# Kernel tuning notes

Hardware: AMD Instinct MI355X
Metric: run time of the kernel (lower is better)

## Reference

```python
import jax, jax.numpy as jnp
import numpy as np

B, S, E, H, D, NE, R = 2, 2048, 2048, 16, 128, 8, 16
HALF = D // 2
THETA = 10000.0


def setup_inputs() -> dict:
    key = jax.random.key(0)
    ks = jax.random.split(key, 18)

    def w(k, shape, fan_in):
        return jax.random.normal(k, shape, jnp.float32) / np.float32(np.sqrt(fan_in))

    inp = {
        "x": jax.random.normal(ks[0], (B, S, E), jnp.float32),
        "expert_mask": jax.random.uniform(ks[1], (B, S, NE), dtype=jnp.float32),
    }
    for i, n in enumerate(("q", "k", "v")):
        inp["W" + n] = w(ks[2 + 3 * i], (H * D, E), E)
        inp["b" + n] = jnp.zeros((H * D,), jnp.float32)
        inp["A" + n] = w(ks[3 + 3 * i], (NE, R, E), E)
        inp["B" + n] = w(ks[4 + 3 * i], (H * D, NE, R), R)
    inp["Wo"] = w(ks[11], (E, H * D), H * D)
    inp["bo"] = jnp.zeros((E,), jnp.float32)
    inp["Ao"] = w(ks[12], (NE, R, H * D), H * D)
    inp["Bo"] = w(ks[13], (E, NE, R), R)
    return inp


def routed_linear(x, W, b, A, Bm, mask):
    """MaybeRoutedLinear: dense base + expert-routed low-rank path gated by mask [B,S,NE]."""
    y = jnp.einsum("bsi,oi->bso", x, W) + b
    h = jnp.einsum("bsi,eri->bser", x, A) * mask[..., None]  # [B,S,NE,R]
    return y + jnp.einsum("bser,oer->bso", h, Bm)


def apply_rope(t):
    """Llama-style rotary embedding. t: [B,S,H,D]."""
    inv_freq = 1.0 / (THETA ** (jnp.arange(0, D, 2, dtype=jnp.float32) / D))  # [D/2]
    freqs = jnp.arange(S, dtype=jnp.float32)[:, None] * inv_freq[None, :]  # [S,D/2]
    cos = jnp.concatenate([jnp.cos(freqs)] * 2, -1)[None, :, None, :]  # [1,S,1,D]
    sin = jnp.concatenate([jnp.sin(freqs)] * 2, -1)[None, :, None, :]
    rot = jnp.concatenate([-t[..., HALF:], t[..., :HALF]], -1)
    return t * cos + rot * sin


def reference(x, expert_mask, Wq, bq, Aq, Bq, Wk, bk, Ak, Bk, Wv, bv, Av, Bv, Wo, bo, Ao, Bo):
    q = routed_linear(x, Wq, bq, Aq, Bq, expert_mask).reshape(B, S, H, D)
    k = routed_linear(x, Wk, bk, Ak, Bk, expert_mask).reshape(B, S, H, D)
    v = routed_linear(x, Wv, bv, Av, Bv, expert_mask).reshape(B, S, H, D)
    q = apply_rope(q)
    k = apply_rope(k)
    scores = jnp.einsum("bqhd,bkhd->bhqk", q, k) / jnp.float32(np.sqrt(D))
    causal = jnp.tril(jnp.ones((S, S), dtype=bool))
    scores = jnp.where(causal[None, None], scores, jnp.finfo(scores.dtype).min)
    probs = jax.nn.softmax(scores, axis=-1)
    o = jnp.einsum("bhqk,bkhd->bqhd", probs, v).reshape(B, S, H * D)
    return routed_linear(o, Wo, bo, Ao, Bo, expert_mask)
```

## Files before the change

### kernel.cpp

```cpp
#include <hip/hip_runtime.h>


#define B_ 2
#define S_ 2048
#define E_ 2048
#define H_ 16
#define D_ 128
#define NE_ 8
#define R_ 16
#define HD_ 2048
#define M_ 4096
#define KL_ 128

typedef unsigned short u16;
typedef unsigned int u32;
typedef __attribute__((ext_vector_type(8))) short bf16x8;
typedef __attribute__((ext_vector_type(4))) float f32x4;

typedef const __attribute__((address_space(1))) void gvoid_t;
typedef __attribute__((address_space(3))) void svoid_t;

__device__ __forceinline__ float bf2f(u16 u) {
    union { u32 i; float f; } v; v.i = ((u32)u) << 16; return v.f;
}
__device__ __forceinline__ u16 f2bf(float f) {
    union { float f; u32 i; } v; v.f = f;
    u32 x = v.i;
    return (u16)((x + 0x7fffu + ((x >> 16) & 1u)) >> 16);
}
__device__ __forceinline__ float ldf(const void* p, size_t i, int f) {
    return f ? ((const float*)p)[i] : bf2f(((const u16*)p)[i]);
}
__device__ __forceinline__ float4 ld4(const void* p, size_t i, int f) {
    if (f) return *(const float4*)((const float*)p + i);
    ushort4 v = *(const ushort4*)((const u16*)p + i);
    return make_float4(bf2f(v.x), bf2f(v.y), bf2f(v.z), bf2f(v.w));
}

__global__ void k_detect(const void* __restrict__ x, int* __restrict__ flags) {
    __shared__ int votes[2];
    int tid = threadIdx.x;
    if (tid < 2) votes[tid] = 0;
    __syncthreads();
    const u32* p = (const u32*)x;
    int bad = 0, tot = 0;
    for (int i = tid; i < 4096; i += 64) {
        u32 lo = p[i] & 0xffffu;
        if (lo) {
            tot++;
            int e = (int)((lo >> 7) & 0xffu);
            if (e < 100 || e > 150) bad++;
        }
    }
    atomicAdd(&votes[0], bad);
    atomicAdd(&votes[1], tot);
    __syncthreads();
    if (tid == 0) flags[0] = (votes[1] > 0 && votes[0] * 10 > votes[1] * 3) ? 1 : 0;
}

__global__ void k_cvt(const void* __restrict__ src, u16* __restrict__ dst, int n,
                      const int* __restrict__ flags) {
    int fin = flags[0];
    int i = (blockIdx.x * 256 + threadIdx.x) * 4;
    if (i >= n) return;
    float4 v = ld4(src, i, fin);
    ushort4 o;
    o.x = f2bf(v.x); o.y = f2bf(v.y); o.z = f2bf(v.z); o.w = f2bf(v.w);
    *(ushort4*)(dst + i) = o;
}

#define NX_  8388608L
#define NA1_ 262144L
#define NW_  4194304L
__global__ void k_cvt_all(
    const void* __restrict__ x,
    const void* __restrict__ Aq, const void* __restrict__ Ak,
    const void* __restrict__ Av, const void* __restrict__ Ao,
    const void* __restrict__ Bq, const void* __restrict__ Bk,
    const void* __restrict__ Bv, const void* __restrict__ Bo,
    const void* __restrict__ Wq, const void* __restrict__ Wk,
    const void* __restrict__ Wv,
    u16* __restrict__ Xb, u16* __restrict__ Acat, u16* __restrict__ Bmcat,
    u16* __restrict__ Wqb, u16* __restrict__ Wkb, u16* __restrict__ Wvb,
    const int* __restrict__ flags) {
    int fin = flags[0];
    long i = (long)(blockIdx.x * 256 + threadIdx.x) * 4;
    const void* src; u16* dst; long off;
    if (i < NX_) { src = x; dst = Xb; off = i; }
    else if (i < NX_ + 4 * NA1_) {
        long j = i - NX_; int p = (int)(j >> 18); off = j & (NA1_ - 1);
        src = (p == 0) ? Aq : (p == 1) ? Ak : (p == 2) ? Av : Ao;
        dst = Acat + (long)p * NA1_;
    } else if (i < NX_ + 8 * NA1_) {
        long j = i - NX_ - 4 * NA1_; int p = (int)(j >> 18); off = j & (NA1_ - 1);
        src = (p == 0) ? Bq : (p == 1) ? Bk : (p == 2) ? Bv : Bo;
        dst = Bmcat + (long)p * NA1_;
    } else {
        long j = i - NX_ - 8 * NA1_; int p = (int)(j / NW_); off = j - (long)p * NW_;
        src = (p == 0) ? Wq : (p == 1) ? Wk : Wv;
        dst = (p == 0) ? Wqb : (p == 1) ? Wkb : Wvb;
    }
    float4 v = ld4(src, off, fin);
    ushort4 o;
    o.x = f2bf(v.x); o.y = f2bf(v.y); o.z = f2bf(v.z); o.w = f2bf(v.w);
    *(ushort4*)(dst + off) = o;
}

#define BM_ 128
#define BN_ 128
#define BK_ 64

__global__ __launch_bounds__(256, 2) void k_gemm_mfma(
    const u16* __restrict__ A, int lda,
    const u16* __restrict__ Bw, int ldb, int K1,
    const u16* __restrict__ A2, int lda2,
    const u16* __restrict__ B2, int K2,
    const void* __restrict__ bias, const void* __restrict__ mask,
    void* __restrict__ C, int ldc, int store_mode,
    const int* __restrict__ flags) {
    __shared__ __align__(16) u16 As[BM_ * BK_];
    __shared__ __align__(16) u16 Bs[BN_ * BK_];
    int fin = flags[0];
    int tid = threadIdx.x;
    int w = tid >> 6, lane = tid & 63;
    int l15 = lane & 15, quad = lane >> 4;
    int wm = w >> 1, wn = w & 1;
    int m0 = blockIdx.y * BM_, n0 = blockIdx.x * BN_;
    int lrow = lane >> 3;
    int lcol = (lane & 7) * 8;

    f32x4 acc[4][4];
#pragma unroll
    for (int mt = 0; mt < 4; mt++)
#pragma unroll
        for (int nt = 0; nt < 4; nt++)
#pragma unroll
            for (int r = 0; r < 4; r++) acc[mt][nt][r] = 0.f;

    int n1 = K1 / BK_, n2 = K2 / BK_;
    int total = n1 + n2;
    for (int it = 0; it < total; it++) {
        const u16 *pa, *pb; int sa, sb, kb;
        if (it < n1) { pa = A;  sa = lda;  pb = Bw; sb = ldb; kb = it * BK_; }
        else         { pa = A2; sa = lda2; pb = B2; sb = K2;  kb = (it - n1) * BK_; }
        __syncthreads();
#pragma unroll
        for (int i = 0; i < 4; i++) {
            int rowb = (w * 4 + i) * 8;
            int r = rowb + lrow;
            __builtin_amdgcn_global_load_lds(
                (gvoid_t*)(pa + (size_t)(m0 + r) * sa + kb + lcol),
                (svoid_t*)(As + rowb * BK_), 16, 0, 0);
            __builtin_amdgcn_global_load_lds(
                (gvoid_t*)(pb + (size_t)(n0 + r) * sb + kb + lcol),
                (svoid_t*)(Bs + rowb * BK_), 16, 0, 0);
        }
        __syncthreads();
#pragma unroll
        for (int kk = 0; kk < 2; kk++) {
            int ko = kk * 32 + quad * 8;
            bf16x8 af[4], bf[4];
#pragma unroll
            for (int mt = 0; mt < 4; mt++)
                af[mt] = *(const bf16x8*)(As + (wm * 64 + mt * 16 + l15) * BK_ + ko);
#pragma unroll
            for (int nt = 0; nt < 4; nt++)
                bf[nt] = *(const bf16x8*)(Bs + (wn * 64 + nt * 16 + l15) * BK_ + ko);
#pragma unroll
            for (int mt = 0; mt < 4; mt++)
#pragma unroll
                for (int nt = 0; nt < 4; nt++)
                    acc[mt][nt] = __builtin_amdgcn_mfma_f32_16x16x32_bf16(
                        af[mt], bf[nt], acc[mt][nt], 0, 0, 0);
        }
    }

#pragma unroll
    for (int mt = 0; mt < 4; mt++) {
#pragma unroll
        for (int r = 0; r < 4; r++) {
            int m = m0 + wm * 64 + mt * 16 + quad * 4 + r;
#pragma unroll
            for (int nt = 0; nt < 4; nt++) {
                int n = n0 + wn * 64 + nt * 16 + l15;
                float v = acc[mt][nt][r];
                if (bias) v += ldf(bias, (size_t)n, fin);
                if (mask) v *= ldf(mask, (size_t)m * NE_ + ((n & 127) >> 4), fin);
                int f32out = (store_mode == 2) ? fin : store_mode;
                if (f32out) ((float*)C)[(size_t)m * ldc + n] = v;
                else        ((u16*)C)[(size_t)m * ldc + n] = f2bf(v);
            }
        }
    }
}

__global__ void k_rope2(u16* __restrict__ Q, u16* __restrict__ K) {
    const int n = M_ * HD_ / 2;
    int idx = blockIdx.x * 256 + threadIdx.x;
    u16* Y = (idx < n) ? Q : K;
    int id = (idx < n) ? idx : idx - n;
    int d2 = id & 63;
    int sh = id >> 6;
    int s = (sh >> 4) & (S_ - 1);
    float inv = powf(10000.f, -(float)d2 * (1.f / 64.f));
    float fr = (float)s * inv;
    float c, sn;
    sincosf(fr, &sn, &c);
    size_t base = ((size_t)sh) << 7;
    float t0 = bf2f(Y[base + d2]);
    float t1 = bf2f(Y[base + d2 + 64]);
    Y[base + d2]      = f2bf(t0 * c - t1 * sn);
    Y[base + d2 + 64] = f2bf(t1 * c + t0 * sn);
}

__global__ void k_transpose_v(const u16* __restrict__ Vb, u16* __restrict__ Vt) {
    __shared__ u16 t[32][33];
    int s0 = blockIdx.x * 32;
    int n0 = blockIdx.y * 32;
    int b  = blockIdx.z;
    int tx = threadIdx.x & 31, ty = threadIdx.x >> 5;
#pragma unroll
    for (int r = 0; r < 4; r++)
        t[ty + r * 8][tx] = Vb[((size_t)(b * S_ + s0 + ty + r * 8)) * HD_ + n0 + tx];
    __syncthreads();
#pragma unroll
    for (int r = 0; r < 4; r++)
        Vt[((size_t)(b * HD_ + n0 + ty + r * 8)) * S_ + s0 + tx] = t[tx][ty + r * 8];
}

#define KS_ST 136
#define VT_ST 72
#define SCALE_ 0.088388347648318447f

__global__ __launch_bounds__(256, 3) void k_flash6(
    const u16* __restrict__ Q, const u16* __restrict__ K,
    const u16* __restrict__ Vt, u16* __restrict__ O) {
    __shared__ __align__(16) u16 Ks[64 * KS_ST];
    __shared__ __align__(16) u16 Vs[128 * VT_ST];
    __shared__ __align__(16) u16 Ps[64 * VT_ST];
    int tid = threadIdx.x;
    int w = tid >> 6, lane = tid & 63;
    int l15 = lane & 15, quad = lane >> 4;
    int bh = blockIdx.y, b = bh >> 4, h = bh & 15;
    int t = 31 - blockIdx.x;
    int q0 = t * 64;

    int krow[4], kd8[4], vd[4], vkg[4];
#pragma unroll
    for (int it = 0; it < 4; it++) {
        int idx = it * 256 + tid;
        krow[it] = idx >> 4; kd8[it] = (idx & 15) * 8;
        vd[it] = idx >> 3;   vkg[it] = (idx & 7) * 8;
    }

    bf16x8 qf[4];
    size_t baseQ = ((size_t)(b * S_ + q0 + w * 16 + l15)) * HD_ + h * D_;
#pragma unroll
    for (int ks = 0; ks < 4; ks++)
        qf[ks] = *(const bf16x8*)(Q + baseQ + ks * 32 + quad * 8);

    f32x4 of[8];
#pragma unroll
    for (int nt = 0; nt < 8; nt++)
#pragma unroll
        for (int r = 0; r < 4; r++) of[nt][r] = 0.f;
    float mreg = -30000.f, lreg = 0.f;
    int qrow = q0 + w * 16 + l15;

    int nch = t + 1;

    bf16x8 kpre[4], vpre[4];
#pragma unroll
    for (int it = 0; it < 4; it++) {
        kpre[it] = *(const bf16x8*)(K + ((size_t)(b * S_ + krow[it])) * HD_ + h * D_ + kd8[it]);
        vpre[it] = *(const bf16x8*)(Vt + ((size_t)(bh * 128 + vd[it])) * S_ + vkg[it]);
    }

    for (int c = 0; c < nch; c++) {
        int k0 = c * 64;
        __syncthreads();
#pragma unroll
        for (int it = 0; it < 4; it++) {
            *(bf16x8*)(Ks + krow[it] * KS_ST + kd8[it]) = kpre[it];
            *(bf16x8*)(Vs + vd[it] * VT_ST + vkg[it]) = vpre[it];
        }
        __syncthreads();
        if (c + 1 < nch) {
            int k1 = k0 + 64;
#pragma unroll
            for (int it = 0; it < 4; it++) {
                kpre[it] = *(const bf16x8*)(K + ((size_t)(b * S_ + k1 + krow[it])) * HD_ + h * D_ + kd8[it]);
                vpre[it] = *(const bf16x8*)(Vt + ((size_t)(bh * 128 + vd[it])) * S_ + k1 + vkg[it]);
            }
        }

        f32x4 sf[4];
#pragma unroll
        for (int nt = 0; nt < 4; nt++)
#pragma unroll
            for (int r = 0; r < 4; r++) sf[nt][r] = 0.f;
#pragma unroll
        for (int ks = 0; ks < 4; ks++) {
            int koff = ks * 32 + quad * 8;
            bf16x8 qa = qf[ks];
#pragma unroll
            for (int nt = 0; nt < 4; nt++) {
                bf16x8 kb = *(const bf16x8*)(Ks + (nt * 16 + l15) * KS_ST + koff);
                sf[nt] = __builtin_amdgcn_mfma_f32_16x16x32_bf16(kb, qa, sf[nt], 0, 0, 0);
            }
        }

#pragma unroll
        for (int nt = 0; nt < 4; nt++) {
            int keyb = k0 + nt * 16 + quad * 4;
#pragma unroll
            for (int r = 0; r < 4; r++) {
                float sv = sf[nt][r] * SCALE_;
                sf[nt][r] = (keyb + r > qrow) ? -30000.f : sv;
            }
        }

        float t0 = fmaxf(fmaxf(sf[0][0], sf[0][1]), fmaxf(sf[0][2], sf[0][3]));
        float t1 = fmaxf(fmaxf(sf[1][0], sf[1][1]), fmaxf(sf[1][2], sf[1][3]));
        float t2 = fmaxf(fmaxf(sf[2][0], sf[2][1]), fmaxf(sf[2][2], sf[2][3]));
        float t3 = fmaxf(fmaxf(sf[3][0], sf[3][1]), fmaxf(sf[3][2], sf[3][3]));
        float cmax = fmaxf(fmaxf(t0, t1), fmaxf(t2, t3));
        cmax = fmaxf(cmax, __shfl_xor(cmax, 16, 64));
        cmax = fmaxf(cmax, __shfl_xor(cmax, 32, 64));
        float mnew = fmaxf(mreg, cmax);
        float a = __expf(mreg - mnew);
        mreg = mnew;
#pragma unroll
        for (int nt = 0; nt < 4; nt++)
#pragma unroll
            for (int r = 0; r < 4; r++)
                sf[nt][r] = __expf(sf[nt][r] - mnew);
        float s0 = (sf[0][0] + sf[0][1]) + (sf[0][2] + sf[0][3]);
        float s1 = (sf[1][0] + sf[1][1]) + (sf[1][2] + sf[1][3]);
        float s2 = (sf[2][0] + sf[2][1]) + (sf[2][2] + sf[2][3]);
        float s3 = (sf[3][0] + sf[3][1]) + (sf[3][2] + sf[3][3]);
        float psum = (s0 + s1) + (s2 + s3);
        psum += __shfl_xor(psum, 16, 64);
        psum += __shfl_xor(psum, 32, 64);
        lreg = lreg * a + psum;

        float al[4];
#pragma unroll
        for (int r = 0; r < 4; r++) al[r] = __shfl(a, quad * 4 + r, 16);

#pragma unroll
        for (int nt = 0; nt < 4; nt++)
#pragma unroll
            for (int r = 0; r < 4; r++)
                Ps[(w * 16 + l15) * VT_ST + nt * 16 + quad * 4 + r] = f2bf(sf[nt][r]);
#pragma unroll
        for (int nt = 0; nt < 8; nt++)
#pragma unroll
            for (int r = 0; r < 4; r++) of[nt][r] *= al[r];

#pragma unroll
        for (int ks2 = 0; ks2 < 2; ks2++) {
            int koff = ks2 * 32 + quad * 8;
            bf16x8 pa = *(const bf16x8*)(Ps + (w * 16 + l15) * VT_ST + koff);
#pragma unroll
            for (int nt = 0; nt < 8; nt++) {
                bf16x8 vb = *(const bf16x8*)(Vs + (nt * 16 + l15) * VT_ST + koff);
                of[nt] = __builtin_amdgcn_mfma_f32_16x16x32_bf16(pa, vb, of[nt], 0, 0, 0);
            }
        }
    }

    float linv = 1.f / lreg;
    float inv[4];
#pragma unroll
    for (int r = 0; r < 4; r++) inv[r] = __shfl(linv, quad * 4 + r, 16);
    int rowb = q0 + w * 16 + quad * 4;
#pragma unroll
    for (int r = 0; r < 4; r++) {
        size_t base = ((size_t)(b * S_ + rowb + r)) * HD_ + h * D_;
#pragma unroll
        for (int nt = 0; nt < 8; nt++)
            O[base + nt * 16 + l15] = f2bf(of[nt][r] * inv[r]);
    }
}

extern "C" void kernel_launch(void* const* d_in, const int* in_sizes, int n_in,
                              void* d_out, int out_size, void* d_ws, size_t ws_size,
                              hipStream_t stream) {
    const void* x    = d_in[0];
    const void* mask = d_in[1];
    const void* Wq = d_in[2];  const void* bq = d_in[3];
    const void* Aq = d_in[4];  const void* Bq = d_in[5];
    const void* Wk = d_in[6];  const void* bk = d_in[7];
    const void* Ak = d_in[8];  const void* Bk = d_in[9];
    const void* Wv = d_in[10]; const void* bv = d_in[11];
    const void* Av = d_in[12]; const void* Bv = d_in[13];
    const void* Wo = d_in[14]; const void* bo = d_in[15];
    const void* Ao = d_in[16]; const void* Bo = d_in[17];

    char* ws = (char*)d_ws;
    const long MB = 1 << 20;
    int* flags = (int*)ws;
    u16* Xb    = (u16*)(ws + 1  * MB);
    u16* Acat  = (u16*)(ws + 17 * MB);
    u16* Bmcat = (u16*)(ws + 19 * MB);
    u16* hg3   = (u16*)(ws + 21 * MB);
    u16* hgo   = (u16*)(ws + 24 * MB);
    u16* Qb    = (u16*)(ws + 25 * MB);
    u16* Kb    = (u16*)(ws + 41 * MB);
    u16* Vb    = (u16*)(ws + 57 * MB);
    u16* Vt    = (u16*)(ws + 73 * MB);
    u16* Wqb   = Kb;
    u16* Wkb   = Vb;
    u16* Wvb   = Vt;
    u16* Wob   = Qb;
    u16* Ob    = Vb;

    k_detect<<<1, 64, 0, stream>>>(x, flags);
    const long NCVT = NX_ + 8 * NA1_ + 3 * NW_;
    k_cvt_all<<<NCVT / 1024, 256, 0, stream>>>(
        x, Aq, Ak, Av, Ao, Bq, Bk, Bv, Bo, Wq, Wk, Wv,
        Xb, Acat, Bmcat, Wqb, Wkb, Wvb, flags);

    k_gemm_mfma<<<dim3(3, M_ / BM_), 256, 0, stream>>>(
        Xb, E_, Acat, E_, E_, nullptr, 0, nullptr, 0,
        nullptr, mask, hg3, 384, 0, flags);

    dim3 gg(HD_ / BN_, M_ / BM_);
    k_gemm_mfma<<<gg, 256, 0, stream>>>(Xb, E_, Wqb, E_, E_, hg3 + 0,   384, Bmcat, KL_,
                                        bq, nullptr, Qb, HD_, 0, flags);
    k_gemm_mfma<<<gg, 256, 0, stream>>>(Xb, E_, Wkb, E_, E_, hg3 + 128, 384, Bmcat + NA1_, KL_,
                                        bk, nullptr, Kb, HD_, 0, flags);
    k_gemm_mfma<<<gg, 256, 0, stream>>>(Xb, E_, Wvb, E_, E_, hg3 + 256, 384, Bmcat + 2 * NA1_, KL_,
                                        bv, nullptr, Vb, HD_, 0, flags);

    k_rope2<<<(M_ * HD_) / 256, 256, 0, stream>>>(Qb, Kb);
    k_transpose_v<<<dim3(S_ / 32, HD_ / 32, B_), 256, 0, stream>>>(Vb, Vt);

    k_flash6<<<dim3(32, 32), 256, 0, stream>>>(Qb, Kb, Vt, Ob);

    k_cvt<<<NW_ / 1024, 256, 0, stream>>>(Wo, Wob, (int)NW_, flags);
    k_gemm_mfma<<<dim3(1, M_ / BM_), 256, 0, stream>>>(
        Ob, HD_, Acat + 3 * NA1_, E_, E_, nullptr, 0, nullptr, 0,
        nullptr, mask, hgo, KL_, 0, flags);
    k_gemm_mfma<<<gg, 256, 0, stream>>>(Ob, HD_, Wob, E_, E_, hgo, KL_, Bmcat + 3 * NA1_, KL_,
                                        bo, nullptr, d_out, HD_, 2, flags);
}
```

Before: 723.3 us.

## Fuse QKV projections into one 256x256-tile GEMM with 4-stage LDS pipeline

Replaces the three separate Q/K/V projection GEMMs with a single launch of a new 256x256-tile, 512-thread MFMA kernel. The kernel reads a concatenated bf16 weight buffer, chooses the per-projection bias and low-rank operands from the column block, and scatters into the Q/K/V outputs. It prefetches 4 stages through direct global-to-LDS loads with explicit vmcnt waits and uses a grouped tile swizzle. The output projection also switches to this kernel. The larger tiles are meant to raise operand reuse and cut launch count, at the cost of about 128KB of LDS per block (so roughly one block per CU) and only 128 blocks for the output GEMM, which may leave many CUs idle.

Result: slower. 798.5 us (+10.4%).

```diff
diff --git a/kernel.cpp b/kernel.cpp
--- a/kernel.cpp
+++ b/kernel.cpp
@@ -81,7 +81,7 @@
     const void* __restrict__ Wq, const void* __restrict__ Wk,
     const void* __restrict__ Wv,
     u16* __restrict__ Xb, u16* __restrict__ Acat, u16* __restrict__ Bmcat,
-    u16* __restrict__ Wqb, u16* __restrict__ Wkb, u16* __restrict__ Wvb,
+    u16* __restrict__ Wcat,
     const int* __restrict__ flags) {
     int fin = flags[0];
     long i = (long)(blockIdx.x * 256 + threadIdx.x) * 4;
@@ -98,7 +98,7 @@
     } else {
         long j = i - NX_ - 8 * NA1_; int p = (int)(j / NW_); off = j - (long)p * NW_;
         src = (p == 0) ? Wq : (p == 1) ? Wk : Wv;
-        dst = (p == 0) ? Wqb : (p == 1) ? Wkb : Wvb;
+        dst = Wcat + (long)p * NW_;
     }
     float4 v = ld4(src, off, fin);
     ushort4 o;
@@ -194,6 +194,130 @@
     }
 }
 
+#define GBM 256
+#define GBN 256
+#define GBK 32
+
+__global__ __launch_bounds__(512, 2) void k_gemm256(
+    const u16* __restrict__ A, int lda,
+    const u16* __restrict__ Bw, int ldb, int K1,
+    const u16* __restrict__ A2, int lda2,
+    const u16* __restrict__ B2, int K2,
+    const void* __restrict__ bias0, const void* __restrict__ bias1,
+    const void* __restrict__ bias2,
+    void* __restrict__ C, int ldc, int store_mode,
+    const int* __restrict__ flags) {
+    __shared__ __align__(16) u16 As[4][GBM * GBK];
+    __shared__ __align__(16) u16 Bs[4][GBN * GBK];
+    int fin = flags[0];
+    int tid = threadIdx.x;
+    int w = tid >> 6, lane = tid & 63;
+    int l15 = lane & 15, quad = lane >> 4;
+    int wm = w >> 2, wn = w & 3;
+
+    int nxt = gridDim.x;
+    int lin = blockIdx.y * gridDim.x + blockIdx.x;
+    int cpx = (gridDim.x * gridDim.y) >> 3;
+    int wg = (lin & 7) * cpx + (lin >> 3);
+    int m0 = (wg / nxt) * GBM;
+    int n0 = (wg % nxt) * GBN;
+
+    int p = (store_mode == 3) ? (n0 >> 11) : 0;
+    const u16* A2p = A2 + p * 128;
+    const u16* B2p = B2 + (long)p * NA1_;
+    int nloc = (store_mode == 3) ? (n0 & 2047) : n0;
+
+    int srow = tid >> 2;
+    int scol = (tid & 3) * 8;
+    int nk1 = K1 >> 5;
+    int NT = nk1 + (K2 >> 5);
+
+    f32x4 acc[8][4];
+#pragma unroll
+    for (int mt = 0; mt < 8; mt++)
+#pragma unroll
+        for (int nt = 0; nt < 4; nt++)
+#pragma unroll
+            for (int r = 0; r < 4; r++) acc[mt][nt][r] = 0.f;
+
+    auto stage = [&](int kt) {
+        const u16 *pa, *pb; int sa, sb, kb, nb;
+        if (kt < nk1) { pa = A;   sa = lda;  pb = Bw;  sb = ldb; kb = kt * GBK; nb = n0; }
+        else          { pa = A2p; sa = lda2; pb = B2p; sb = K2;  kb = (kt - nk1) * GBK; nb = nloc; }
+        int buf = kt & 3;
+#pragma unroll
+        for (int j = 0; j < 2; j++) {
+            __builtin_amdgcn_global_load_lds(
+                (gvoid_t*)(pa + (size_t)(m0 + j * 128 + srow) * sa + kb + scol),
+                (svoid_t*)(&As[buf][(j * 128 + w * 16) * GBK]), 16, 0, 0);
+            __builtin_amdgcn_global_load_lds(
+                (gvoid_t*)(pb + (size_t)(nb + j * 128 + srow) * sb + kb + scol),
+                (svoid_t*)(&Bs[buf][(j * 128 + w * 16) * GBK]), 16, 0, 0);
+        }
+    };
+
+    stage(0);
+    if (NT > 1) stage(1);
+    if (NT > 2) stage(2);
+
+    for (int kt = 0; kt < NT; kt++) {
+        int buf = kt & 3;
+        if (kt + 3 < NT) {
+            stage(kt + 3);
+            asm volatile("s_waitcnt vmcnt(12)" ::: "memory");
+        } else {
+            int rem = NT - 1 - kt;
+            if (rem >= 2)      asm volatile("s_waitcnt vmcnt(8)" ::: "memory");
+            else if (rem == 1) asm volatile("s_waitcnt vmcnt(4)" ::: "memory");
+            else               asm volatile("s_waitcnt vmcnt(0)" ::: "memory");
+        }
+        __builtin_amdgcn_s_barrier();
+        __builtin_amdgcn_sched_barrier(0);
+
+        bf16x8 af[8], bfr[4];
+#pragma unroll
+        for (int mt = 0; mt < 8; mt++)
+            af[mt] = *(const bf16x8*)(&As[buf][(wm * 128 + mt * 16 + l15) * GBK + quad * 8]);
+#pragma unroll
+        for (int nt = 0; nt < 4; nt++)
+            bfr[nt] = *(const bf16x8*)(&Bs[buf][(wn * 64 + nt * 16 + l15) * GBK + quad * 8]);
+
+        __builtin_amdgcn_s_setprio(1);
+#pragma unroll
+        for (int mt = 0; mt < 8; mt++)
+#pragma unroll
+            for (int nt = 0; nt < 4; nt++)
+                acc[mt][nt] = __builtin_amdgcn_mfma_f32_16x16x32_bf16(
+                    af[mt], bfr[nt], acc[mt][nt], 0, 0, 0);
+        __builtin_amdgcn_s_setprio(0);
+
+        __builtin_amdgcn_s_barrier();
+        __builtin_amdgcn_sched_barrier(0);
+    }
+
+    const void* bp = (store_mode == 3) ? (p == 0 ? bias0 : p == 1 ? bias1 : bias2)
+                                       : bias0;
+#pragma unroll
+    for (int mt = 0; mt < 8; mt++) {
+#pragma unroll
+        for (int r = 0; r < 4; r++) {
+            int m = m0 + wm * 128 + mt * 16 + quad * 4 + r;
+#pragma unroll
+            for (int nt = 0; nt < 4; nt++) {
+                int n = n0 + wn * 64 + nt * 16 + l15;
+                float v = acc[mt][nt][r];
+                if (bp) v += ldf(bp, (size_t)(n & 2047), fin);
+                if (store_mode == 3) {
+                    ((u16*)C)[(size_t)p * 8388608 + (size_t)m * 2048 + (n & 2047)] = f2bf(v);
+                } else {
+                    if (fin) ((float*)C)[(size_t)m * ldc + n] = v;
+                    else     ((u16*)C)[(size_t)m * ldc + n] = f2bf(v);
+                }
+            }
+        }
+    }
+}
+
 __global__ void k_rope2(u16* __restrict__ Q, u16* __restrict__ K) {
     const int n = M_ * HD_ / 2;
     int idx = blockIdx.x * 256 + threadIdx.x;
@@ -410,9 +534,7 @@
     u16* Kb    = (u16*)(ws + 41 * MB);
     u16* Vb    = (u16*)(ws + 57 * MB);
     u16* Vt    = (u16*)(ws + 73 * MB);
-    u16* Wqb   = Kb;
-    u16* Wkb   = Vb;
-    u16* Wvb   = Vt;
+    u16* Wcat  = (u16*)(ws + 73 * MB);
     u16* Wob   = Qb;
     u16* Ob    = Vb;
 
@@ -420,19 +542,15 @@
     const long NCVT = NX_ + 8 * NA1_ + 3 * NW_;
     k_cvt_all<<<NCVT / 1024, 256, 0, stream>>>(
         x, Aq, Ak, Av, Ao, Bq, Bk, Bv, Bo, Wq, Wk, Wv,
-        Xb, Acat, Bmcat, Wqb, Wkb, Wvb, flags);
+        Xb, Acat, Bmcat, Wcat, flags);
 
     k_gemm_mfma<<<dim3(3, M_ / BM_), 256, 0, stream>>>(
         Xb, E_, Acat, E_, E_, nullptr, 0, nullptr, 0,
         nullptr, mask, hg3, 384, 0, flags);
 
-    dim3 gg(HD_ / BN_, M_ / BM_);
-    k_gemm_mfma<<<gg, 256, 0, stream>>>(Xb, E_, Wqb, E_, E_, hg3 + 0,   384, Bmcat, KL_,
-                                        bq, nullptr, Qb, HD_, 0, flags);
-    k_gemm_mfma<<<gg, 256, 0, stream>>>(Xb, E_, Wkb, E_, E_, hg3 + 128, 384, Bmcat + NA1_, KL_,
-                                        bk, nullptr, Kb, HD_, 0, flags);
-    k_gemm_mfma<<<gg, 256, 0, stream>>>(Xb, E_, Wvb, E_, E_, hg3 + 256, 384, Bmcat + 2 * NA1_, KL_,
-                                        bv, nullptr, Vb, HD_, 0, flags);
+    k_gemm256<<<dim3(6144 / GBN, M_ / GBM), 512, 0, stream>>>(
+        Xb, E_, Wcat, E_, E_, hg3, 384, Bmcat, KL_,
+        bq, bk, bv, Qb, HD_, 3, flags);
 
     k_rope2<<<(M_ * HD_) / 256, 256, 0, stream>>>(Qb, Kb);
     k_transpose_v<<<dim3(S_ / 32, HD_ / 32, B_), 256, 0, stream>>>(Vb, Vt);
@@ -443,6 +561,7 @@
     k_gemm_mfma<<<dim3(1, M_ / BM_), 256, 0, stream>>>(
         Ob, HD_, Acat + 3 * NA1_, E_, E_, nullptr, 0, nullptr, 0,
         nullptr, mask, hgo, KL_, 0, flags);
-    k_gemm_mfma<<<gg, 256, 0, stream>>>(Ob, HD_, Wob, E_, E_, hgo, KL_, Bmcat + 3 * NA1_, KL_,
-                                        bo, nullptr, d_out, HD_, 2, flags);
-}
+    k_gemm256<<<dim3(HD_ / GBN, M_ / GBM), 512, 0, stream>>>(
+        Ob, HD_, Wob, E_, E_, hgo, KL_, Bmcat + 3 * NA1_, KL_,
+        bo, nullptr, nullptr, d_out, HD_, 2, flags);
+}
```
